# Performance work log

Hardware: AMD Instinct MI355X
Metric: run time of the kernel (lower is better)

Reference implementation:

```python
import jax, jax.numpy as jnp
import numpy as np

K_TARGETS = 15  # hardcoded k in _select_targets
N_CLASSES = 8


def setup_inputs() -> dict:
    key = jax.random.key(0)
    k1, k2, k3 = jax.random.split(key, 3)
    n, p, d = 128, 512, 64
    return {
        "segment_center": jax.random.normal(k1, (n, d), dtype=jnp.float32),
        "outputs": jax.random.normal(k2, (n, p, d), dtype=jnp.float32),
        "label_inds": jax.random.randint(k3, (n, p), 0, N_CLASSES),
    }


def reference(segment_center, outputs, label_inds):
    # segment_center: [n, d]; outputs: [n, p, d]; label_inds: [n, p] int
    n, p, d = outputs.shape
    labels = label_inds.reshape(n, p)
    same = labels[:, :, None] == labels[:, None, :]          # [n, p, p] same-label mask

    # squared distance of each point to its segment center: cdist(...)^2
    dist_c = jnp.sum((outputs - segment_center[:, None, :]) ** 2, axis=-1)  # [n, p]

    # _select_targets: dd[n,i,j] = dist_c[n,i], masked to +inf where labels differ,
    # topk smallest over j -> k same-label target-neighbor indices per point.
    dd = jnp.where(same, dist_c[:, :, None], jnp.inf)        # [n, p, p]
    _, target_neighbors = jax.lax.top_k(-dd, K_TARGETS)      # [n, p, K] smallest

    # squared center-distance of each target neighbor (intended gather in forward)
    gathered = dist_c[jnp.arange(n)[:, None, None], target_neighbors]  # [n, p, K]

    furthest = gathered.max(axis=2)                          # [n, p]
    margin_radii = 1.0 + furthest                            # per-point margin
    pull_loss = gathered.sum()

    # _find_impostors: per-segment margin = 1 + max center-dist over all gathered
    # target neighbors; impostor (n,i,j) iff label_i != label_j and
    # dist_c[n,i] < margin_seg[n]. Hinge term depends only on (n,i), so sum the
    # hinge weighted by the count of different-label j (avoids nonzero/gather).
    margin_seg = 1.0 + gathered.max(axis=(1, 2))             # [n]
    diff_count = (p - same.sum(axis=2)).astype(outputs.dtype)  # [n, p] #{j: label_j != label_i}
    is_impostor = (dist_c < margin_seg[:, None]).astype(outputs.dtype)  # [n, p]
    hinge = jnp.maximum(margin_radii - dist_c, 0.0)          # [n, p]
    push_loss = jnp.sum(diff_count * is_impostor * hinge)

    return (pull_loss + push_loss) / (n * p)
```

## Files before the change

### kernel.cpp

```cpp
#include <hip/hip_runtime.h>
#include <math.h>

constexpr int NSEG = 128;
constexpr int P    = 512;
constexpr int D    = 64;
constexpr int KT   = 15;
constexpr int NCLS = 8;

__global__ __launch_bounds__(256) void dist_kernel(
    const float* __restrict__ center,
    const float* __restrict__ outputs,
    float* __restrict__ dist)
{
    const int seg     = blockIdx.x >> 2;
    const int quarter = blockIdx.x & 3;
    const int t   = threadIdx.x;
    const int sub = t & 15;
    const int pg  = t >> 4;

    const float4* c4 = reinterpret_cast<const float4*>(center);
    const float4  cf = c4[seg * 16 + sub];

    const float4* o4 = reinterpret_cast<const float4*>(outputs);
    const int pt_base = quarter * 128;

    #pragma unroll
    for (int it = 0; it < 8; ++it) {
        const int pt = pt_base + it * 16 + pg;
        float4 v = o4[((size_t)seg * P + pt) * 16 + sub];
        float dx = v.x - cf.x;
        float dy = v.y - cf.y;
        float dz = v.z - cf.z;
        float dw = v.w - cf.w;
        float acc = dx * dx + dy * dy + dz * dz + dw * dw;
        acc += __shfl_xor(acc, 1);
        acc += __shfl_xor(acc, 2);
        acc += __shfl_xor(acc, 4);
        acc += __shfl_xor(acc, 8);
        if (sub == 0) dist[seg * P + pt] = acc;
    }
}

__global__ __launch_bounds__(512, 1) void combine_kernel(
    const float* __restrict__ dist,
    const int*   __restrict__ labels,
    float* __restrict__ out)
{
    __shared__ float s_dist[P];
    __shared__ int   s_lab[P];
    __shared__ float s_S[NCLS];
    __shared__ float s_M[NCLS];
    __shared__ int   s_cnt[NCLS];
    __shared__ float s_hb[NCLS];
    __shared__ float s_dc[NCLS];
    __shared__ float s_margin;
    __shared__ float s_pull;
    __shared__ float s_wsum[8];

    const int seg  = blockIdx.x;
    const int tid  = threadIdx.x;
    const int lane = tid & 63;
    const int wave = tid >> 6;

    s_lab[tid]  = labels[seg * P + tid];
    s_dist[tid] = dist[seg * P + tid];
    __syncthreads();

    {
        const int c = wave;
        float S = 0.0f;
        float M = -INFINITY;
        int taken = 0;
        int total = 0;
        for (int j = 0; j < 8; ++j) {
            const int pos = j * 64 + lane;
            const bool pred = (s_lab[pos] == c);
            const unsigned long long mask = __ballot(pred);
            const int cnt  = __popcll(mask);
            const int rank = __popcll(mask & ((1ull << lane) - 1ull));
            const bool sel = pred && (taken + rank < KT);
            float vs = sel ? s_dist[pos] : 0.0f;
            float vm = sel ? s_dist[pos] : -INFINITY;
            #pragma unroll
            for (int m = 1; m < 64; m <<= 1) {
                vs += __shfl_xor(vs, m);
                vm = fmaxf(vm, __shfl_xor(vm, m));
            }
            S += vs;
            M = fmaxf(M, vm);
            total += cnt;
            taken += cnt;
            if (taken > KT) taken = KT;
        }
        if (total < KT) {
            const int need = KT - total;
            int t2 = 0;
            for (int j = 0; j < 8 && t2 < need; ++j) {
                const int pos = j * 64 + lane;
                const bool pred = (s_lab[pos] != c);
                const unsigned long long mask = __ballot(pred);
                const int cnt  = __popcll(mask);
                const int rank = __popcll(mask & ((1ull << lane) - 1ull));
                const bool sel = pred && (t2 + rank < need);
                float vs = sel ? s_dist[pos] : 0.0f;
                float vm = sel ? s_dist[pos] : -INFINITY;
                #pragma unroll
                for (int m = 1; m < 64; m <<= 1) {
                    vs += __shfl_xor(vs, m);
                    vm = fmaxf(vm, __shfl_xor(vm, m));
                }
                S += vs;
                M = fmaxf(M, vm);
                t2 += cnt;
                if (t2 > need) t2 = need;
            }
        }
        if (lane == 0) {
            s_S[c]   = S;
            s_M[c]   = M;
            s_cnt[c] = total;
        }
    }
    __syncthreads();

    if (tid == 0) {
        float margin = -INFINITY;
        float pull = 0.0f;
        for (int c = 0; c < NCLS; ++c) {
            if (s_cnt[c] > 0) margin = fmaxf(margin, s_M[c]);
            pull += (float)s_cnt[c] * s_S[c];
            s_hb[c] = 1.0f + s_M[c];
            s_dc[c] = (float)(P - s_cnt[c]);
        }
        s_margin = 1.0f + margin;
        s_pull = pull;
    }
    __syncthreads();

    {
        const float dv = s_dist[tid];
        const int   c  = s_lab[tid];
        const float h  = fmaxf(s_hb[c] - dv, 0.0f);
        float v = (dv < s_margin) ? s_dc[c] * h : 0.0f;
        #pragma unroll
        for (int m = 1; m < 64; m <<= 1) v += __shfl_xor(v, m);
        if (lane == 0) s_wsum[wave] = v;
    }
    __syncthreads();

    if (tid == 0) {
        float t = s_pull;
        #pragma unroll
        for (int w = 0; w < 8; ++w) t += s_wsum[w];
        atomicAdd(out, t * (1.0f / ((float)NSEG * (float)P)));
    }
}

extern "C" void kernel_launch(void* const* d_in, const int* in_sizes, int n_in,
                              void* d_out, int out_size, void* d_ws, size_t ws_size,
                              hipStream_t stream) {
    const float* center  = (const float*)d_in[0];
    const float* outputs = (const float*)d_in[1];
    const int*   labels  = (const int*)d_in[2];
    float* out  = (float*)d_out;
    float* dist = (float*)d_ws;

    hipMemsetAsync(out, 0, sizeof(float), stream);
    dist_kernel<<<dim3(NSEG * 4), dim3(256), 0, stream>>>(center, outputs, dist);
    combine_kernel<<<dim3(NSEG), dim3(512), 0, stream>>>(dist, labels, out);
}
```

Baseline: 76.69 us.

## Fuse distance and combine kernels with last-block-per-segment atomic counters

Merges the distance kernel and the per-segment combine kernel into one launch. Each block atomically bumps a per-segment counter, and the last of the four blocks for a segment does the class selection and hinge reduction using 256 threads. A global counter then lets the last segment write the final output instead of using a memset plus atomicAdd on out. This removes one kernel launch and its serialization gap, at the cost of extra atomics and fences and a tail with only a quarter of blocks active.

Result: slower. 134.5 us (+75.4%).

```diff
diff --git a/kernel.cpp b/kernel.cpp
--- a/kernel.cpp
+++ b/kernel.cpp
@@ -7,9 +7,15 @@
 constexpr int KT   = 15;
 constexpr int NCLS = 8;
 
-__global__ __launch_bounds__(256) void dist_kernel(
+
+__global__ __launch_bounds__(256) void lmnn_fused(
     const float* __restrict__ center,
     const float* __restrict__ outputs,
+    const int*   __restrict__ labels,
+    float* __restrict__ out,
+    int*   __restrict__ counters,
+    int*   __restrict__ gcount,
+    float* __restrict__ gaccum,
     float* __restrict__ dist)
 {
     const int seg     = blockIdx.x >> 2;
@@ -20,7 +26,6 @@
 
     const float4* c4 = reinterpret_cast<const float4*>(center);
     const float4  cf = c4[seg * 16 + sub];
-
     const float4* o4 = reinterpret_cast<const float4*>(outputs);
     const int pt_base = quarter * 128;
 
@@ -39,13 +44,15 @@
         acc += __shfl_xor(acc, 8);
         if (sub == 0) dist[seg * P + pt] = acc;
     }
-}
 
-__global__ __launch_bounds__(512, 1) void combine_kernel(
-    const float* __restrict__ dist,
-    const int*   __restrict__ labels,
-    float* __restrict__ out)
-{
+    __threadfence();
+    __syncthreads();
+    __shared__ int s_old;
+    if (t == 0) s_old = atomicAdd(&counters[seg], 1);
+    __syncthreads();
+    if (s_old != 3) return;
+    __threadfence();
+
     __shared__ float s_dist[P];
     __shared__ int   s_lab[P];
     __shared__ float s_S[NCLS];
@@ -55,19 +62,19 @@
     __shared__ float s_dc[NCLS];
     __shared__ float s_margin;
     __shared__ float s_pull;
-    __shared__ float s_wsum[8];
+    __shared__ float s_wsum[4];
 
-    const int seg  = blockIdx.x;
-    const int tid  = threadIdx.x;
-    const int lane = tid & 63;
-    const int wave = tid >> 6;
-
-    s_lab[tid]  = labels[seg * P + tid];
-    s_dist[tid] = dist[seg * P + tid];
+    s_lab[t]        = labels[seg * P + t];
+    s_lab[t + 256]  = labels[seg * P + t + 256];
+    s_dist[t]       = dist[seg * P + t];
+    s_dist[t + 256] = dist[seg * P + t + 256];
     __syncthreads();
 
-    {
-        const int c = wave;
+    const int lane = t & 63;
+    const int wave = t >> 6;
+
+    for (int ci = 0; ci < 2; ++ci) {
+        const int c = wave + ci * 4;
         float S = 0.0f;
         float M = -INFINITY;
         int taken = 0;
@@ -123,7 +130,7 @@
     }
     __syncthreads();
 
-    if (tid == 0) {
+    if (t == 0) {
         float margin = -INFINITY;
         float pull = 0.0f;
         for (int c = 0; c < NCLS; ++c) {
@@ -138,21 +145,31 @@
     __syncthreads();
 
     {
-        const float dv = s_dist[tid];
-        const int   c  = s_lab[tid];
-        const float h  = fmaxf(s_hb[c] - dv, 0.0f);
-        float v = (dv < s_margin) ? s_dc[c] * h : 0.0f;
+        float v = 0.0f;
+        #pragma unroll
+        for (int k = 0; k < 2; ++k) {
+            const int pos = t + k * 256;
+            const float dv = s_dist[pos];
+            const int   c  = s_lab[pos];
+            const float h  = fmaxf(s_hb[c] - dv, 0.0f);
+            v += (dv < s_margin) ? s_dc[c] * h : 0.0f;
+        }
         #pragma unroll
         for (int m = 1; m < 64; m <<= 1) v += __shfl_xor(v, m);
         if (lane == 0) s_wsum[wave] = v;
     }
     __syncthreads();
 
-    if (tid == 0) {
-        float t = s_pull;
-        #pragma unroll
-        for (int w = 0; w < 8; ++w) t += s_wsum[w];
-        atomicAdd(out, t * (1.0f / ((float)NSEG * (float)P)));
+    if (t == 0) {
+        float tt = s_pull + s_wsum[0] + s_wsum[1] + s_wsum[2] + s_wsum[3];
+        atomicAdd(gaccum, tt);
+        __threadfence();
+        const int o2 = atomicAdd(gcount, 1);
+        if (o2 == NSEG - 1) {
+            __threadfence();
+            const float tot = atomicAdd(gaccum, 0.0f);
+            out[0] = tot * (1.0f / ((float)NSEG * (float)P));
+        }
     }
 }
 
@@ -162,10 +179,14 @@
     const float* center  = (const float*)d_in[0];
     const float* outputs = (const float*)d_in[1];
     const int*   labels  = (const int*)d_in[2];
-    float* out  = (float*)d_out;
-    float* dist = (float*)d_ws;
+    float* out = (float*)d_out;
 
-    hipMemsetAsync(out, 0, sizeof(float), stream);
-    dist_kernel<<<dim3(NSEG * 4), dim3(256), 0, stream>>>(center, outputs, dist);
-    combine_kernel<<<dim3(NSEG), dim3(512), 0, stream>>>(dist, labels, out);
+    int*   counters = (int*)d_ws;
+    int*   gcount   = counters + NSEG;
+    float* gaccum   = (float*)(counters + NSEG + 1);
+    float* dist     = (float*)((char*)d_ws + 1024);
+
+    hipMemsetAsync(d_ws, 0, 1024, stream);
+    lmnn_fused<<<dim3(NSEG * 4), dim3(256), 0, stream>>>(
+        center, outputs, labels, out, counters, gcount, gaccum, dist);
 }
```
